# Performance work log

Measured on AMD Instinct MI355X. Metric: run time of the kernel, lower is better.

## Reference

```python
import jax, jax.numpy as jnp
import numpy as np

N = 100000
E = 1600000
IN_C, HID_C, OUT_C = 128, 128, 64


def setup_inputs() -> dict:
    key = jax.random.key(0)
    ks = jax.random.split(key, 8)
    x = jax.random.normal(ks[0], (N, IN_C), dtype=jnp.float32)
    edge_index = jax.random.randint(ks[1], (2, E), 0, N, dtype=jnp.int64)
    # Glorot-ish init for the 3 GCNConv linear weights + zero biases (PyG default)
    def glorot(k, fan_in, fan_out):
        s = jnp.sqrt(6.0 / (fan_in + fan_out))
        return jax.random.uniform(k, (fan_in, fan_out), jnp.float32, -s, s)
    return {
        "x": x,
        "edge_index": edge_index,
        "W1": glorot(ks[2], IN_C, HID_C), "b1": jnp.zeros((HID_C,), jnp.float32),
        "W2": glorot(ks[3], HID_C, HID_C), "b2": jnp.zeros((HID_C,), jnp.float32),
        "W3": glorot(ks[4], HID_C, OUT_C), "b3": jnp.zeros((OUT_C,), jnp.float32),
    }


def _gcn_norm(edge_index, num_nodes):
    # add self loops, compute D^-1/2 (A+I) D^-1/2 edge coefficients (PyG gcn_norm)
    loop = jnp.arange(num_nodes, dtype=edge_index.dtype)
    src = jnp.concatenate([edge_index[0], loop])  # [E+N]
    dst = jnp.concatenate([edge_index[1], loop])
    w = jnp.ones_like(src, dtype=jnp.float32)
    deg = jax.ops.segment_sum(w, dst, num_segments=num_nodes)
    dinv = jnp.where(deg > 0, jax.lax.rsqrt(deg), 0.0)
    norm = dinv[src] * dinv[dst]  # [E+N]
    return src, dst, norm


def _gcn_layer(x, src, dst, norm, W, b, num_nodes):
    h = x @ W                                   # [N, out]
    msg = h[src] * norm[:, None]                # gather + scale, [E+N, out]
    agg = jax.ops.segment_sum(msg, dst, num_segments=num_nodes)  # scatter-add
    return agg + b


def reference(x, edge_index, W1, b1, W2, b2, W3, b3):
    src, dst, norm = _gcn_norm(edge_index, N)
    h = jax.nn.relu(_gcn_layer(x, src, dst, norm, W1, b1, N))
    h = jax.nn.relu(_gcn_layer(h, src, dst, norm, W2, b2, N))
    h = _gcn_layer(h, src, dst, norm, W3, b3, N)
    return jax.nn.log_softmax(h, axis=-1)  # [N, OUT_C]
```

## Files before the change

kernel.cpp:

```cpp
#include <hip/hip_runtime.h>
#include <hip/hip_bf16.h>


constexpr int N_NODES = 100000;
constexpr int E_EDGES = 1600000;
constexpr int NB = (N_NODES + 127) / 128;
constexpr int BCAP = 2560;
constexpr int CHUNK = 8192;
constexpr int NCHUNK = (E_EDGES + CHUNK - 1) / CHUNK;

typedef short bf16x8 __attribute__((ext_vector_type(8)));
typedef float f32x4 __attribute__((ext_vector_type(4)));

__device__ __forceinline__ unsigned short f2bf(float f) {
    unsigned u = __float_as_uint(f);
    unsigned r = (u + 0x7fff + ((u >> 16) & 1)) >> 16;
    return (unsigned short)r;
}
__device__ __forceinline__ float bf_lo(unsigned u) { return __uint_as_float(u << 16); }
__device__ __forceinline__ float bf_hi(unsigned u) { return __uint_as_float(u & 0xffff0000u); }

__global__ void detect_kernel(const int* __restrict__ ei32, int* __restrict__ flag) {
    if (threadIdx.x == 0) {
        int ok64 = 1;
#pragma unroll
        for (int i = 1; i < 64; i += 2) ok64 &= (ei32[i] == 0);
        *flag = ok64;
    }
}

__device__ __forceinline__ int get_idx(const void* ei, int use64, long long pos) {
    if (use64) return (int)((const long long*)ei)[pos];
    return ((const int*)ei)[pos];
}

__global__ __launch_bounds__(256) void scatter_direct(
    const void* __restrict__ ei, const int* __restrict__ flag,
    int* __restrict__ cursorPad, unsigned* __restrict__ pairs) {
    __shared__ int h[NB];
    __shared__ int base[NB];
    __shared__ unsigned dstb[CHUNK];
    const int t = threadIdx.x;
    const int use64 = *flag;
    const int e0 = blockIdx.x * CHUNK;
    const int e1 = min(E_EDGES, e0 + CHUNK);

    for (int i = t; i < NB; i += 256) h[i] = 0;
    __syncthreads();
    for (int e = e0 + t; e < e1; e += 256) {
        unsigned d = (unsigned)get_idx(ei, use64, (long long)E_EDGES + e);
        dstb[e - e0] = d;
        atomicAdd(&h[d >> 7], 1);
    }
    __syncthreads();
    for (int i = t; i < NB; i += 256) {
        int c = h[i];
        if (c) base[i] = atomicAdd(&cursorPad[i * 16], c);
        h[i] = 0;
    }
    __syncthreads();
    for (int e = e0 + t; e < e1; e += 256) {
        unsigned s = (unsigned)get_idx(ei, use64, e);
        unsigned d = dstb[e - e0];
        int b = d >> 7;
        int r = base[b] + atomicAdd(&h[b], 1);
        if (r < BCAP) pairs[(unsigned)b * BCAP + r] = (s << 7) | (d & 127u);
    }
}

__global__ __launch_bounds__(256) void fine_sort_kernel(
    const unsigned* __restrict__ pairs, const int* __restrict__ cursorPad,
    int* __restrict__ csr, int* __restrict__ rowptr, int* __restrict__ deg,
    float* __restrict__ dinv) {
    __shared__ int h[128];
    __shared__ int rp[128];
    __shared__ int sc[128];
    const int t = threadIdx.x;
    const int b = blockIdx.x;
    const int base = b * BCAP;
    const int cnt = min(cursorPad[b * 16], BCAP);

    if (t < 128) h[t] = 0;
    __syncthreads();
    for (int i = t; i < cnt; i += 256) {
        unsigned p = pairs[base + i];
        atomicAdd(&h[p & 127u], 1);
    }
    __syncthreads();
    int v = (t < 128) ? h[t] : 0;
    if (t < 128) sc[t] = v;
    __syncthreads();
    int incl = v;
    for (int off = 1; off < 128; off <<= 1) {
        int add = (t >= off && t < 128) ? sc[t - off] : 0;
        __syncthreads();
        if (t < 128) {
            incl += add;
            sc[t] = incl;
        }
        __syncthreads();
    }
    if (t < 128) {
        rp[t] = incl - v;
        int node = b * 128 + t;
        if (node < N_NODES) {
            rowptr[node] = base + incl - v;
            deg[node] = v;
            dinv[node] = rsqrtf((float)(v + 1));
        }
        h[t] = 0;
    }
    __syncthreads();
    for (int i = t; i < cnt; i += 256) {
        unsigned p = pairs[base + i];
        int l = (int)(p & 127u);
        int r = atomicAdd(&h[l], 1);
        csr[base + rp[l] + r] = (int)(p >> 7);
    }
}

__global__ void prep_wt_kernel(const float* __restrict__ W1, const float* __restrict__ W2,
                               const float* __restrict__ W3,
                               unsigned short* __restrict__ WT1,
                               unsigned short* __restrict__ WT2,
                               unsigned short* __restrict__ WT3) {
    const int b = blockIdx.x;
    const float* W = (b == 0) ? W1 : (b == 1) ? W2 : W3;
    unsigned short* WT = (b == 0) ? WT1 : (b == 1) ? WT2 : WT3;
    const int COUT = (b == 2) ? 64 : 128;
    for (int i = threadIdx.x; i < COUT * 128; i += blockDim.x) {
        int c = i >> 7;
        int k = i & 127;
        WT[c * 128 + k] = f2bf(W[k * COUT + c]);
    }
}

template <int COUT>
__global__ __launch_bounds__(256) void gemm_mfma(const float* __restrict__ X,
                                                 const unsigned short* __restrict__ WT,
                                                 const float* __restrict__ dinv,
                                                 unsigned short* __restrict__ H) {
    constexpr int NT = COUT / 16;
    __shared__ short Albs[64 * 128];
    __shared__ short Wlds[COUT * 128];

    const int t = threadIdx.x;
    const int row0 = blockIdx.x * 64;

    for (int i = t; i < COUT * 16; i += 256) {
        int n = i >> 4, k8 = i & 15;
        bf16x8 v = *(const bf16x8*)&WT[n * 128 + k8 * 8];
        *(bf16x8*)&Wlds[(k8 * COUT + n) * 8] = v;
    }
    for (int i = t; i < 1024; i += 256) {
        int m = i >> 4, k8 = i & 15;
        int gr = min(row0 + m, N_NODES - 1);
        const float* p = &X[(size_t)gr * 128 + k8 * 8];
        float4 f0 = *(const float4*)p;
        float4 f1 = *(const float4*)(p + 4);
        bf16x8 v;
        v[0] = (short)f2bf(f0.x); v[1] = (short)f2bf(f0.y);
        v[2] = (short)f2bf(f0.z); v[3] = (short)f2bf(f0.w);
        v[4] = (short)f2bf(f1.x); v[5] = (short)f2bf(f1.y);
        v[6] = (short)f2bf(f1.z); v[7] = (short)f2bf(f1.w);
        int u = ((m >> 4) * 16 + (k8 >> 2) * 4 + (k8 & 3)) * 16 + (m & 15);
        *(bf16x8*)&Albs[u * 8] = v;
    }
    __syncthreads();

    const int lane = t & 63;
    const int wv = t >> 6;
    const int l15 = lane & 15;
    const int quad = lane >> 4;

    f32x4 acc[NT];
#pragma unroll
    for (int ct = 0; ct < NT; ct++) acc[ct] = (f32x4){0.f, 0.f, 0.f, 0.f};

#pragma unroll
    for (int kcg = 0; kcg < 4; kcg++) {
        bf16x8 a = *(const bf16x8*)&Albs[((wv * 16 + kcg * 4 + quad) * 16 + l15) * 8];
#pragma unroll
        for (int ct = 0; ct < NT; ct++) {
            bf16x8 b = *(const bf16x8*)&Wlds[((kcg * 4 + quad) * COUT + ct * 16 + l15) * 8];
            acc[ct] = __builtin_amdgcn_mfma_f32_16x16x32_bf16(a, b, acc[ct], 0, 0, 0);
        }
    }

    const int m0 = row0 + wv * 16;
#pragma unroll
    for (int r = 0; r < 4; r++) {
        int m = m0 + quad * 4 + r;
        if (m < N_NODES) {
            float dv = dinv[m];
#pragma unroll
            for (int ct = 0; ct < NT; ct++)
                H[(size_t)m * COUT + ct * 16 + l15] = f2bf(acc[ct][r] * dv);
        } else if (m == N_NODES) {
#pragma unroll
            for (int ct = 0; ct < NT; ct++)
                H[(size_t)m * COUT + ct * 16 + l15] = 0;
        }
    }
}

__global__ __launch_bounds__(256) void aggregate128_pair(
    const unsigned short* __restrict__ Hb, const int* __restrict__ rowptr,
    const int* __restrict__ deg, const int* __restrict__ csr,
    const float* __restrict__ dinv, const float* __restrict__ bias,
    float* __restrict__ out) {
    const int lane = threadIdx.x & 63;
    const int wv = threadIdx.x >> 6;
    const int li = lane & 31;
    const int half = lane >> 5;
    const int n = blockIdx.x * 8 + wv * 2 + half;
    const unsigned li8 = (unsigned)li * 8u;
    const char* Hc = (const char*)Hb;

    uint2 s = *(const uint2*)(Hc + (unsigned)n * 256u + li8);
    float a0 = bf_lo(s.x), a1 = bf_hi(s.x), a2 = bf_lo(s.y), a3 = bf_hi(s.y);

    const int start = rowptr[n];
    const int dc = deg[n];
    const int dmax = max(dc, __shfl_xor(dc, 32));

    for (int eb = 0; eb < dmax; eb += 32) {
        int myidx = N_NODES;
        if (eb + li < dc) myidx = csr[start + eb + li];
        const int jmax = min(32, dmax - eb);
        int j = 0;
        for (; j + 8 <= jmax; j += 8) {
            int idx[8];
            uint2 u[8];
#pragma unroll
            for (int q = 0; q < 8; q++) idx[q] = __shfl(myidx, j + q, 32);
#pragma unroll
            for (int q = 0; q < 8; q++)
                u[q] = *(const uint2*)(Hc + (((unsigned)idx[q] << 8) + li8));
#pragma unroll
            for (int q = 0; q < 8; q++) {
                a0 += bf_lo(u[q].x); a1 += bf_hi(u[q].x);
                a2 += bf_lo(u[q].y); a3 += bf_hi(u[q].y);
            }
        }
        for (; j + 4 <= jmax; j += 4) {
            int idx[4];
            uint2 u[4];
#pragma unroll
            for (int q = 0; q < 4; q++) idx[q] = __shfl(myidx, j + q, 32);
#pragma unroll
            for (int q = 0; q < 4; q++)
                u[q] = *(const uint2*)(Hc + (((unsigned)idx[q] << 8) + li8));
#pragma unroll
            for (int q = 0; q < 4; q++) {
                a0 += bf_lo(u[q].x); a1 += bf_hi(u[q].x);
                a2 += bf_lo(u[q].y); a3 += bf_hi(u[q].y);
            }
        }
        for (; j < jmax; j++) {
            int i0 = __shfl(myidx, j, 32);
            uint2 u0 = *(const uint2*)(Hc + (((unsigned)i0 << 8) + li8));
            a0 += bf_lo(u0.x); a1 += bf_hi(u0.x);
            a2 += bf_lo(u0.y); a3 += bf_hi(u0.y);
        }
    }

    const float dn = dinv[n];
    float4 bv = *(const float4*)((const char*)bias + li * 16);
    float4 o;
    o.x = fmaxf(a0 * dn + bv.x, 0.f);
    o.y = fmaxf(a1 * dn + bv.y, 0.f);
    o.z = fmaxf(a2 * dn + bv.z, 0.f);
    o.w = fmaxf(a3 * dn + bv.w, 0.f);
    *(float4*)((char*)out + (size_t)n * 512 + li * 16) = o;
}

__global__ __launch_bounds__(256) void aggregate64_lsm_pair(
    const unsigned short* __restrict__ Hb, const int* __restrict__ rowptr,
    const int* __restrict__ deg, const int* __restrict__ csr,
    const float* __restrict__ dinv, const float* __restrict__ bias,
    float* __restrict__ out) {
    const int lane = threadIdx.x & 63;
    const int wv = threadIdx.x >> 6;
    const int li = lane & 31;
    const int half = lane >> 5;
    const int n = blockIdx.x * 8 + wv * 2 + half;
    const unsigned li4 = (unsigned)li * 4u;
    const char* Hc = (const char*)Hb;

    unsigned s = *(const unsigned*)(Hc + (unsigned)n * 128u + li4);
    float a0 = bf_lo(s), a1 = bf_hi(s);

    const int start = rowptr[n];
    const int dc = deg[n];
    const int dmax = max(dc, __shfl_xor(dc, 32));

    for (int eb = 0; eb < dmax; eb += 32) {
        int myidx = N_NODES;
        if (eb + li < dc) myidx = csr[start + eb + li];
        const int jmax = min(32, dmax - eb);
        int j = 0;
        for (; j + 8 <= jmax; j += 8) {
            int idx[8];
            unsigned u[8];
#pragma unroll
            for (int q = 0; q < 8; q++) idx[q] = __shfl(myidx, j + q, 32);
#pragma unroll
            for (int q = 0; q < 8; q++)
                u[q] = *(const unsigned*)(Hc + (((unsigned)idx[q] << 7) + li4));
#pragma unroll
            for (int q = 0; q < 8; q++) { a0 += bf_lo(u[q]); a1 += bf_hi(u[q]); }
        }
        for (; j + 4 <= jmax; j += 4) {
            int idx[4];
            unsigned u[4];
#pragma unroll
            for (int q = 0; q < 4; q++) idx[q] = __shfl(myidx, j + q, 32);
#pragma unroll
            for (int q = 0; q < 4; q++)
                u[q] = *(const unsigned*)(Hc + (((unsigned)idx[q] << 7) + li4));
#pragma unroll
            for (int q = 0; q < 4; q++) { a0 += bf_lo(u[q]); a1 += bf_hi(u[q]); }
        }
        for (; j < jmax; j++) {
            int i0 = __shfl(myidx, j, 32);
            unsigned u0 = *(const unsigned*)(Hc + (((unsigned)i0 << 7) + li4));
            a0 += bf_lo(u0); a1 += bf_hi(u0);
        }
    }

    const float dn = dinv[n];
    float2 bv = *(const float2*)((const char*)bias + li * 8);
    float v0 = a0 * dn + bv.x;
    float v1 = a1 * dn + bv.y;

    float m = fmaxf(v0, v1);
#pragma unroll
    for (int off = 16; off; off >>= 1) m = fmaxf(m, __shfl_xor(m, off));
    float e = expf(v0 - m) + expf(v1 - m);
#pragma unroll
    for (int off = 16; off; off >>= 1) e += __shfl_xor(e, off);
    float lse = m + logf(e);
    float2 o = make_float2(v0 - lse, v1 - lse);
    *(float2*)((char*)out + (size_t)n * 256 + li * 8) = o;
}

extern "C" void kernel_launch(void* const* d_in, const int* in_sizes, int n_in,
                              void* d_out, int out_size, void* d_ws, size_t ws_size,
                              hipStream_t stream) {
    const float* x = (const float*)d_in[0];
    const void* ei = d_in[1];
    const float* W1 = (const float*)d_in[2];
    const float* b1 = (const float*)d_in[3];
    const float* W2 = (const float*)d_in[4];
    const float* b2 = (const float*)d_in[5];
    const float* W3 = (const float*)d_in[6];
    const float* b3 = (const float*)d_in[7];
    float* out = (float*)d_out;

    char* w = (char*)d_ws;
    size_t off = 0;
    auto take = [&](size_t bytes) {
        char* p = w + off;
        off = (off + bytes + 255) & ~(size_t)255;
        return p;
    };
    int* flag = (int*)take(4);
    int* cursorPad = (int*)take((size_t)NB * 64);
    int* deg = (int*)take((size_t)N_NODES * 4);
    int* rowptr = (int*)take((size_t)N_NODES * 4);
    float* dinv = (float*)take((size_t)N_NODES * 4);
    int* csr = (int*)take((size_t)NB * BCAP * 4);
    unsigned short* WT1 = (unsigned short*)take(128 * 128 * 2);
    unsigned short* WT2 = (unsigned short*)take(128 * 128 * 2);
    unsigned short* WT3 = (unsigned short*)take(64 * 128 * 2);
    unsigned short* A = (unsigned short*)take((size_t)(N_NODES + 1) * 128 * 2);
    float* B = (float*)take((size_t)N_NODES * 128 * 4);
    unsigned* pairs = (unsigned*)A;

    hipMemsetAsync(cursorPad, 0, (size_t)NB * 64, stream);
    detect_kernel<<<1, 64, 0, stream>>>((const int*)ei, flag);
    prep_wt_kernel<<<3, 256, 0, stream>>>(W1, W2, W3, WT1, WT2, WT3);
    scatter_direct<<<NCHUNK, 256, 0, stream>>>(ei, flag, cursorPad, pairs);
    fine_sort_kernel<<<NB, 256, 0, stream>>>(pairs, cursorPad, csr, rowptr, deg, dinv);

    const int gg = (N_NODES + 63) / 64 + 1;
    const int gagg = N_NODES / 8;

    gemm_mfma<128><<<gg, 256, 0, stream>>>(x, WT1, dinv, A);
    aggregate128_pair<<<gagg, 256, 0, stream>>>(A, rowptr, deg, csr, dinv, b1, B);
    gemm_mfma<128><<<gg, 256, 0, stream>>>(B, WT2, dinv, A);
    aggregate128_pair<<<gagg, 256, 0, stream>>>(A, rowptr, deg, csr, dinv, b2, B);
    gemm_mfma<64><<<gg, 256, 0, stream>>>(B, WT3, dinv, A);
    aggregate64_lsm_pair<<<gagg, 256, 0, stream>>>(A, rowptr, deg, csr, dinv, b3, out);
}
```

Before: 370.5 us.

## Sort nodes by degree for aggregation and store intermediates in bf16

```diff
diff --git a/kernel.cpp b/kernel.cpp
--- a/kernel.cpp
+++ b/kernel.cpp
@@ -19,19 +19,39 @@
 }
 __device__ __forceinline__ float bf_lo(unsigned u) { return __uint_as_float(u << 16); }
 __device__ __forceinline__ float bf_hi(unsigned u) { return __uint_as_float(u & 0xffff0000u); }
-
-__global__ void detect_kernel(const int* __restrict__ ei32, int* __restrict__ flag) {
-    if (threadIdx.x == 0) {
-        int ok64 = 1;
-#pragma unroll
-        for (int i = 1; i < 64; i += 2) ok64 &= (ei32[i] == 0);
-        *flag = ok64;
-    }
+__device__ __forceinline__ unsigned pack2bf(float lo, float hi) {
+    return (unsigned)f2bf(lo) | ((unsigned)f2bf(hi) << 16);
 }
 
 __device__ __forceinline__ int get_idx(const void* ei, int use64, long long pos) {
     if (use64) return (int)((const long long*)ei)[pos];
     return ((const int*)ei)[pos];
+}
+
+__global__ void prep_wt_kernel(const float* __restrict__ W1, const float* __restrict__ W2,
+                               const float* __restrict__ W3,
+                               unsigned short* __restrict__ WT1,
+                               unsigned short* __restrict__ WT2,
+                               unsigned short* __restrict__ WT3,
+                               const int* __restrict__ ei32, int* __restrict__ flag) {
+    const int b = blockIdx.x;
+    if (b == 3) {
+        if (threadIdx.x == 0) {
+            int ok64 = 1;
+#pragma unroll
+            for (int i = 1; i < 64; i += 2) ok64 &= (ei32[i] == 0);
+            *flag = ok64;
+        }
+        return;
+    }
+    const float* W = (b == 0) ? W1 : (b == 1) ? W2 : W3;
+    unsigned short* WT = (b == 0) ? WT1 : (b == 1) ? WT2 : WT3;
+    const int COUT = (b == 2) ? 64 : 128;
+    for (int i = threadIdx.x; i < COUT * 128; i += blockDim.x) {
+        int c = i >> 7;
+        int k = i & 127;
+        WT[c * 128 + k] = f2bf(W[k * COUT + c]);
+    }
 }
 
 __global__ __launch_bounds__(256) void scatter_direct(
@@ -119,27 +139,64 @@
     }
 }
 
-__global__ void prep_wt_kernel(const float* __restrict__ W1, const float* __restrict__ W2,
-                               const float* __restrict__ W3,
-                               unsigned short* __restrict__ WT1,
-                               unsigned short* __restrict__ WT2,
-                               unsigned short* __restrict__ WT3) {
-    const int b = blockIdx.x;
-    const float* W = (b == 0) ? W1 : (b == 1) ? W2 : W3;
-    unsigned short* WT = (b == 0) ? WT1 : (b == 1) ? WT2 : WT3;
-    const int COUT = (b == 2) ? 64 : 128;
-    for (int i = threadIdx.x; i < COUT * 128; i += blockDim.x) {
-        int c = i >> 7;
-        int k = i & 127;
-        WT[c * 128 + k] = f2bf(W[k * COUT + c]);
+__global__ __launch_bounds__(256) void deg_hist_kernel(const int* __restrict__ deg,
+                                                       int* __restrict__ degHistPad) {
+    __shared__ int lh[64];
+    const int t = threadIdx.x;
+    if (t < 64) lh[t] = 0;
+    __syncthreads();
+    int n = blockIdx.x * 256 + t;
+    if (n < N_NODES) atomicAdd(&lh[min(deg[n], 63)], 1);
+    __syncthreads();
+    if (t < 64 && lh[t]) atomicAdd(&degHistPad[t * 16], lh[t]);
+}
+
+__global__ void scan_bins_kernel(int* __restrict__ degHistPad) {
+    const int t = threadIdx.x;
+    int v = degHistPad[t * 16];
+    int incl = v;
+#pragma unroll
+    for (int off = 1; off < 64; off <<= 1) {
+        int o = __shfl_up(incl, off);
+        if (t >= off) incl += o;
+    }
+    degHistPad[t * 16] = incl - v;
+}
+
+__global__ __launch_bounds__(256) void build_perm_kernel(
+    const int* __restrict__ deg, const int* __restrict__ rowptr,
+    const float* __restrict__ dinv, int* __restrict__ degCursorPad,
+    int4* __restrict__ nodeinfo) {
+    __shared__ int lh[64];
+    __shared__ int lbase[64];
+    const int t = threadIdx.x;
+    if (t < 64) lh[t] = 0;
+    __syncthreads();
+    const int n = blockIdx.x * 256 + t;
+    int bin = 0, dv = 0;
+    if (n < N_NODES) {
+        dv = deg[n];
+        bin = min(dv, 63);
+        atomicAdd(&lh[bin], 1);
+    }
+    __syncthreads();
+    if (t < 64) {
+        int c = lh[t];
+        lbase[t] = c ? atomicAdd(&degCursorPad[t * 16], c) : 0;
+        lh[t] = 0;
+    }
+    __syncthreads();
+    if (n < N_NODES) {
+        int r = atomicAdd(&lh[bin], 1);
+        nodeinfo[lbase[bin] + r] = make_int4(rowptr[n], dv, __float_as_int(dinv[n]), n);
     }
 }
 
 template <int COUT>
-__global__ __launch_bounds__(256) void gemm_mfma(const float* __restrict__ X,
-                                                 const unsigned short* __restrict__ WT,
-                                                 const float* __restrict__ dinv,
-                                                 unsigned short* __restrict__ H) {
+__global__ __launch_bounds__(256) void gemm_mfma_f32(const float* __restrict__ X,
+                                                     const unsigned short* __restrict__ WT,
+                                                     const float* __restrict__ dinv,
+                                                     unsigned short* __restrict__ H) {
     constexpr int NT = COUT / 16;
     __shared__ short Albs[64 * 128];
     __shared__ short Wlds[COUT * 128];
@@ -204,24 +261,89 @@
     }
 }
 
+template <int COUT>
+__global__ __launch_bounds__(256) void gemm_mfma_bf16(const unsigned short* __restrict__ X,
+                                                      const unsigned short* __restrict__ WT,
+                                                      const float* __restrict__ dinv,
+                                                      unsigned short* __restrict__ H) {
+    constexpr int NT = COUT / 16;
+    __shared__ short Albs[64 * 128];
+    __shared__ short Wlds[COUT * 128];
+
+    const int t = threadIdx.x;
+    const int row0 = blockIdx.x * 64;
+
+    for (int i = t; i < COUT * 16; i += 256) {
+        int n = i >> 4, k8 = i & 15;
+        bf16x8 v = *(const bf16x8*)&WT[n * 128 + k8 * 8];
+        *(bf16x8*)&Wlds[(k8 * COUT + n) * 8] = v;
+    }
+    for (int i = t; i < 1024; i += 256) {
+        int m = i >> 4, k8 = i & 15;
+        int gr = min(row0 + m, N_NODES - 1);
+        bf16x8 v = *(const bf16x8*)&X[(size_t)gr * 128 + k8 * 8];
+        int u = ((m >> 4) * 16 + (k8 >> 2) * 4 + (k8 & 3)) * 16 + (m & 15);
+        *(bf16x8*)&Albs[u * 8] = v;
+    }
+    __syncthreads();
+
+    const int lane = t & 63;
+    const int wv = t >> 6;
+    const int l15 = lane & 15;
+    const int quad = lane >> 4;
+
+    f32x4 acc[NT];
+#pragma unroll
+    for (int ct = 0; ct < NT; ct++) acc[ct] = (f32x4){0.f, 0.f, 0.f, 0.f};
+
+#pragma unroll
+    for (int kcg = 0; kcg < 4; kcg++) {
+        bf16x8 a = *(const bf16x8*)&Albs[((wv * 16 + kcg * 4 + quad) * 16 + l15) * 8];
+#pragma unroll
+        for (int ct = 0; ct < NT; ct++) {
+            bf16x8 b = *(const bf16x8*)&Wlds[((kcg * 4 + quad) * COUT + ct * 16 + l15) * 8];
+            acc[ct] = __builtin_amdgcn_mfma_f32_16x16x32_bf16(a, b, acc[ct], 0, 0, 0);
+        }
+    }
+
+    const int m0 = row0 + wv * 16;
+#pragma unroll
+    for (int r = 0; r < 4; r++) {
+        int m = m0 + quad * 4 + r;
+        if (m < N_NODES) {
+            float dv = dinv[m];
+#pragma unroll
+            for (int ct = 0; ct < NT; ct++)
+                H[(size_t)m * COUT + ct * 16 + l15] = f2bf(acc[ct][r] * dv);
+        } else if (m == N_NODES) {
+#pragma unroll
+            for (int ct = 0; ct < NT; ct++)
+                H[(size_t)m * COUT + ct * 16 + l15] = 0;
+        }
+    }
+}
+
 __global__ __launch_bounds__(256) void aggregate128_pair(
-    const unsigned short* __restrict__ Hb, const int* __restrict__ rowptr,
-    const int* __restrict__ deg, const int* __restrict__ csr,
-    const float* __restrict__ dinv, const float* __restrict__ bias,
-    float* __restrict__ out) {
+    const unsigned short* __restrict__ Hb, const int4* __restrict__ nodeinfo,
+    const int* __restrict__ csr, const float* __restrict__ bias,
+    unsigned short* __restrict__ out) {
     const int lane = threadIdx.x & 63;
     const int wv = threadIdx.x >> 6;
     const int li = lane & 31;
     const int half = lane >> 5;
-    const int n = blockIdx.x * 8 + wv * 2 + half;
+    const int gi = blockIdx.x * 8 + wv * 2 + half;
     const unsigned li8 = (unsigned)li * 8u;
     const char* Hc = (const char*)Hb;
 
-    uint2 s = *(const uint2*)(Hc + (unsigned)n * 256u + li8);
+    const int4 info = nodeinfo[gi];
+    const int start = info.x;
+    const int dc = info.y;
+    const float dn = __int_as_float(info.z);
+    const int n = info.w;
+
+    uint2 s = *(const uint2*)(Hc + (size_t)n * 256u + li8);
     float a0 = bf_lo(s.x), a1 = bf_hi(s.x), a2 = bf_lo(s.y), a3 = bf_hi(s.y);
 
-    const int start = rowptr[n];
-    const int dc = deg[n];
     const int dmax = max(dc, __shfl_xor(dc, 32));
 
     for (int eb = 0; eb < dmax; eb += 32) {
@@ -265,34 +387,34 @@
         }
     }
 
-    const float dn = dinv[n];
     float4 bv = *(const float4*)((const char*)bias + li * 16);
-    float4 o;
-    o.x = fmaxf(a0 * dn + bv.x, 0.f);
-    o.y = fmaxf(a1 * dn + bv.y, 0.f);
-    o.z = fmaxf(a2 * dn + bv.z, 0.f);
-    o.w = fmaxf(a3 * dn + bv.w, 0.f);
-    *(float4*)((char*)out + (size_t)n * 512 + li * 16) = o;
+    uint2 o;
+    o.x = pack2bf(fmaxf(a0 * dn + bv.x, 0.f), fmaxf(a1 * dn + bv.y, 0.f));
+    o.y = pack2bf(fmaxf(a2 * dn + bv.z, 0.f), fmaxf(a3 * dn + bv.w, 0.f));
+    *(uint2*)((char*)out + (size_t)n * 256 + li * 8) = o;
 }
 
 __global__ __launch_bounds__(256) void aggregate64_lsm_pair(
-    const unsigned short* __restrict__ Hb, const int* __restrict__ rowptr,
-    const int* __restrict__ deg, const int* __restrict__ csr,
-    const float* __restrict__ dinv, const float* __restrict__ bias,
+    const unsigned short* __restrict__ Hb, const int4* __restrict__ nodeinfo,
+    const int* __restrict__ csr, const float* __restrict__ bias,
     float* __restrict__ out) {
     const int lane = threadIdx.x & 63;
     const int wv = threadIdx.x >> 6;
     const int li = lane & 31;
     const int half = lane >> 5;
-    const int n = blockIdx.x * 8 + wv * 2 + half;
+    const int gi = blockIdx.x * 8 + wv * 2 + half;
     const unsigned li4 = (unsigned)li * 4u;
     const char* Hc = (const char*)Hb;
 
-    unsigned s = *(const unsigned*)(Hc + (unsigned)n * 128u + li4);
+    const int4 info = nodeinfo[gi];
+    const int start = info.x;
+    const int dc = info.y;
+    const float dn = __int_as_float(info.z);
+    const int n = info.w;
+
+    unsigned s = *(const unsigned*)(Hc + (size_t)n * 128u + li4);
     float a0 = bf_lo(s), a1 = bf_hi(s);
 
-    const int start = rowptr[n];
-    const int dc = deg[n];
     const int dmax = max(dc, __shfl_xor(dc, 32));
 
     for (int eb = 0; eb < dmax; eb += 32) {
@@ -329,7 +451,6 @@
         }
     }
 
-    const float dn = dinv[n];
     float2 bv = *(const float2*)((const char*)bias + li * 8);
     float v0 = a0 * dn + bv.x;
     float v1 = a1 * dn + bv.y;
@@ -366,31 +487,36 @@
         return p;
     };
     int* flag = (int*)take(4);
-    int* cursorPad = (int*)take((size_t)NB * 64);
+    int* cursorPad = (int*)take((size_t)NB * 64 + 64 * 64);
+    int* degHistPad = cursorPad + NB * 16;
     int* deg = (int*)take((size_t)N_NODES * 4);
     int* rowptr = (int*)take((size_t)N_NODES * 4);
     float* dinv = (float*)take((size_t)N_NODES * 4);
     int* csr = (int*)take((size_t)NB * BCAP * 4);
+    int4* nodeinfo = (int4*)take((size_t)N_NODES * 16);
     unsigned short* WT1 = (unsigned short*)take(128 * 128 * 2);
     unsigned short* WT2 = (unsigned short*)take(128 * 128 * 2);
     unsigned short* WT3 = (unsigned short*)take(64 * 128 * 2);
     unsigned short* A = (unsigned short*)take((size_t)(N_NODES + 1) * 128 * 2);
-    float* B = (float*)take((size_t)N_NODES * 128 * 4);
+    unsigned short* B = (unsigned short*)take((size_t)N_NODES * 128 * 2);
     unsigned* pairs = (unsigned*)A;
 
-    hipMemsetAsync(cursorPad, 0, (size_t)NB * 64, stream);
-    detect_kernel<<<1, 64, 0, stream>>>((const int*)ei, flag);
-    prep_wt_kernel<<<3, 256, 0, stream>>>(W1, W2, W3, WT1, WT2, WT3);
+    hipMemsetAsync(cursorPad, 0, (size_t)NB * 64 + 64 * 64, stream);
+    prep_wt_kernel<<<4, 256, 0, stream>>>(W1, W2, W3, WT1, WT2, WT3, (const int*)ei, flag);
     scatter_direct<<<NCHUNK, 256, 0, stream>>>(ei, flag, cursorPad, pairs);
     fine_sort_kernel<<<NB, 256, 0, stream>>>(pairs, cursorPad, csr, rowptr, deg, dinv);
+    deg_hist_kernel<<<(N_NODES + 255) / 256, 256, 0, stream>>>(deg, degHistPad);
+    scan_bins_kernel<<<1, 64, 0, stream>>>(degHistPad);
+    build_perm_kernel<<<(N_NODES + 255) / 256, 256, 0, stream>>>(deg, rowptr, dinv,
+                                                                 degHistPad, nodeinfo);
 
     const int gg = (N_NODES + 63) / 64 + 1;
     const int gagg = N_NODES / 8;
 
-    gemm_mfma<128><<<gg, 256, 0, stream>>>(x, WT1, dinv, A);
-    aggregate128_pair<<<gagg, 256, 0, stream>>>(A, rowptr, deg, csr, dinv, b1, B);
-    gemm_mfma<128><<<gg, 256, 0, stream>>>(B, WT2, dinv, A);
-    aggregate128_pair<<<gagg, 256, 0, stream>>>(A, rowptr, deg, csr, dinv, b2, B);
-    gemm_mfma<64><<<gg, 256, 0, stream>>>(B, WT3, dinv, A);
-    aggregate64_lsm_pair<<<gagg, 256, 0, stream>>>(A, rowptr, deg, csr, dinv, b3, out);
-}
+    gemm_mfma_f32<128><<<gg, 256, 0, stream>>>(x, WT1, dinv, A);
+    aggregate128_pair<<<gagg, 256, 0, stream>>>(A, nodeinfo, csr, b1, B);
+    gemm_mfma_bf16<128><<<gg, 256, 0, stream>>>(B, WT2, dinv, A);
+    aggregate128_pair<<<gagg, 256, 0, stream>>>(A, nodeinfo, csr, b2, B);
+    gemm_mfma_bf16<64><<<gg, 256, 0, stream>>>(B, WT3, dinv, A);
+    aggregate64_lsm_pair<<<gagg, 256, 0, stream>>>(A, nodeinfo, csr, b3, out);
+}
```

Result: slower. 383.8 us (+3.6%).
